# Performance work log

Hardware: AMD Instinct MI355X
Metric: run time of the kernel (lower is better)

## Reference

```python
import jax, jax.numpy as jnp
import numpy as np

SEQ, BATCH = 1024, 128
HIDDEN, EMBED, VOCAB = 2048, 512, 50257
EULER_STEP = 0.01
DIFFUSION = 0.001


def setup_inputs() -> dict:
    key = jax.random.key(0)
    ks = jax.random.split(key, 8)
    sqrt_k = 1.0 / np.sqrt(HIDDEN)
    inp = {
        "input_ids": jax.random.randint(ks[0], (SEQ, BATCH), 0, VOCAB),
        "h_init": jax.random.normal(ks[1], (BATCH, HIDDEN), dtype=jnp.float32),
        "embedding": jax.random.normal(ks[2], (VOCAB, EMBED), dtype=jnp.float32),
        "W_in": jax.random.uniform(ks[3], (HIDDEN, EMBED), jnp.float32, -sqrt_k, sqrt_k),
        "W_h": jax.random.uniform(ks[4], (HIDDEN, HIDDEN), jnp.float32, -sqrt_k, sqrt_k),
        "bias": jax.random.uniform(ks[5], (HIDDEN,), jnp.float32, -sqrt_k, sqrt_k),
        "fc_w": jax.random.uniform(ks[6], (VOCAB, HIDDEN), jnp.float32, -sqrt_k, sqrt_k),
        "fc_b": jax.random.uniform(ks[7], (VOCAB,), jnp.float32, -sqrt_k, sqrt_k),
        "temperature": 1,
    }
    return inp


def reference(input_ids, h_init, embedding, W_in, W_h, bias, fc_w, fc_b, temperature):
    # embed: [S, B, E]
    x = embedding[input_ids]
    # precompute input projection for all steps: [S, B, H]
    xin = jnp.einsum("sbe,he->sbh", x, W_in) + bias
    # effective antisymmetric transition matrix with diffusion
    W_eff = W_h - W_h.T - DIFFUSION * jnp.eye(HIDDEN, dtype=W_h.dtype)

    def step(h, u):
        # F.linear(h, W_eff) == h @ W_eff.T
        h = h + EULER_STEP * (h @ W_eff.T + u)
        return h, None

    h_final, _ = jax.lax.scan(step, h_init, xin)
    logits = (h_final @ fc_w.T + fc_b) / temperature
    return jax.nn.softmax(logits, axis=1)
```

## Files before the change

kernel.cpp:

```cpp
#include <hip/hip_runtime.h>
#include <hip/hip_bf16.h>


typedef _Float16 half8  __attribute__((ext_vector_type(8)));
typedef _Float16 half4h __attribute__((ext_vector_type(4)));
typedef float    f32x4  __attribute__((ext_vector_type(4)));
typedef unsigned int u32;

#define SEQ_    1024
#define BATCH_  128
#define HID_    2048
#define EMB_    512
#define VOC_    50257

__device__ __forceinline__ float decode_temp(const void* tp) {
  int bits = *(const int*)tp;
  float f = __int_as_float(bits);
  if (!(f > 1e-6f && f < 1e6f)) f = (float)bits;
  return f;
}

__device__ __forceinline__ void gl_lds16(const _Float16* g, _Float16* l) {
  __builtin_amdgcn_global_load_lds(
      (const __attribute__((address_space(1))) u32*)g,
      (__attribute__((address_space(3))) u32*)l, 16, 0, 0);
}

__global__ void gather_x_k(const int* __restrict__ ids, const float* __restrict__ embf,
                           _Float16* __restrict__ Xg) {
  const int sb = blockIdx.x * 4 + (threadIdx.x >> 6);
  const int lane = threadIdx.x & 63;
  const int s = sb >> 7, b = sb & 127;
  const int q = s >> 5, r = s & 31;
  const int id = ids[sb];
  const float* src = embf + (size_t)id * EMB_ + lane * 8;
  const f32x4 v0 = *(const f32x4*)src, v1 = *(const f32x4*)(src + 4);
  half8 h = { (_Float16)v0[0], (_Float16)v0[1], (_Float16)v0[2], (_Float16)v0[3],
              (_Float16)v1[0], (_Float16)v1[1], (_Float16)v1[2], (_Float16)v1[3] };
  const size_t drow = ((size_t)q * 128 + b) * 32 + r;
  *(half8*)(Xg + drow * EMB_ + lane * 8) = h;
}

__global__ void prep_R_k(const float* __restrict__ Wh, float* __restrict__ R32,
                         _Float16* __restrict__ R16, _Float16* __restrict__ RT0) {
  __shared__ float tA[64][65], tB[64][65];
  const int bi = blockIdx.y * 64, bj = blockIdx.x * 64;
  const int tx = threadIdx.x & 63, ty = threadIdx.x >> 6;
#pragma unroll
  for (int p = 0; p < 16; ++p) {
    int r = ty + p * 4;
    tA[r][tx] = Wh[(size_t)(bi + r) * HID_ + bj + tx];
    tB[r][tx] = Wh[(size_t)(bj + r) * HID_ + bi + tx];
  }
  __syncthreads();
#pragma unroll
  for (int p = 0; p < 16; ++p) {
    int r = ty + p * 4;
    int i = bi + r, j = bj + tx;
    float v = 0.64f * (tB[tx][r] - tA[r][tx]);
    if (i == j) v = -6.4e-4f;
    size_t idx = (size_t)i * HID_ + j;
    R32[idx] = v;
    R16[idx] = (_Float16)v;
    RT0[idx] = (_Float16)((i == j) ? v : -v);
  }
}

__global__ void copy_win_qt_k(const float* __restrict__ Win, _Float16* __restrict__ QT) {
  int t = blockIdx.x * 256 + threadIdx.x;
  int n = t / (EMB_ / 4), c4 = (t % (EMB_ / 4)) * 4;
  const f32x4 v = *(const f32x4*)(Win + (size_t)n * EMB_ + c4);
  half4h h = { (_Float16)v[0], (_Float16)v[1], (_Float16)v[2], (_Float16)v[3] };
  *(half4h*)(QT + (size_t)n * 16384 + 31 * EMB_ + c4) = h;
}

__global__ void transpose_f2h_k(const float* __restrict__ src, int ldsrc,
                                _Float16* __restrict__ dst, int lddst) {
  __shared__ float t[64][68];
  const int x0 = blockIdx.x * 64, y0 = blockIdx.y * 64;
  const int tid = threadIdx.x;
  const int xc = (tid & 15) * 4, ry = tid >> 4;
#pragma unroll
  for (int p = 0; p < 4; ++p) {
    int row = ry + p * 16;
    const f32x4 v = *(const f32x4*)(src + (size_t)(y0 + row) * ldsrc + x0 + xc);
    *(f32x4*)&t[row][xc] = v;
  }
  __syncthreads();
#pragma unroll
  for (int p = 0; p < 4; ++p) {
    int r2 = ry + p * 16;
    half4h h = { (_Float16)t[xc][r2], (_Float16)t[xc + 1][r2],
                 (_Float16)t[xc + 2][r2], (_Float16)t[xc + 3][r2] };
    *(half4h*)(dst + (size_t)(x0 + r2) * lddst + y0 + xc) = h;
  }
}

__global__ void transpose_q_k(const _Float16* __restrict__ Qst, int firstslot,
                              _Float16* __restrict__ QT) {
  __shared__ _Float16 t[64][72];
  const int slot = firstslot + blockIdx.z;
  const _Float16* src = Qst + (size_t)slot * (EMB_ * HID_);
  const int dc0 = (31 - slot) * EMB_;
  const int x0 = blockIdx.x * 64, y0 = blockIdx.y * 64;
  const int tid = threadIdx.x;
  const int xc = (tid & 7) * 8, ry = tid >> 3;
#pragma unroll
  for (int p = 0; p < 2; ++p) {
    int row = ry + p * 32;
    *(half8*)&t[row][xc] = *(const half8*)(src + (size_t)(y0 + row) * HID_ + x0 + xc);
  }
  __syncthreads();
#pragma unroll
  for (int p = 0; p < 2; ++p) {
    int r2 = ry + p * 32;
    half8 h = { t[xc][r2],     t[xc + 1][r2], t[xc + 2][r2], t[xc + 3][r2],
                t[xc + 4][r2], t[xc + 5][r2], t[xc + 6][r2], t[xc + 7][r2] };
    *(half8*)(QT + (size_t)(x0 + r2) * 16384 + dc0 + y0 + xc) = h;
  }
}

__global__ void gvec_part_k(const float* __restrict__ g, const float* __restrict__ R32,
                            float* __restrict__ gp) {
  const int j = blockIdx.x * 256 + threadIdx.x;
  const int i0 = blockIdx.y * 64;
  float s = 0.f;
#pragma unroll 4
  for (int i = 0; i < 64; ++i) s += g[i0 + i] * R32[(size_t)(i0 + i) * HID_ + j];
  gp[(size_t)blockIdx.y * HID_ + j] = s;
}
__global__ void gvec_red_k(const float* __restrict__ g, const float* __restrict__ gp,
                           float* __restrict__ gout) {
  const int j = blockIdx.x * 256 + threadIdx.x;
  float s = 0.f;
#pragma unroll
  for (int ib = 0; ib < 32; ++ib) s += gp[(size_t)ib * HID_ + j];
  gout[j] = 2.f * g[j] + s * (1.0f / 64.0f);
}

template<int BM, int BN, int BK, int WM, int WN, int ASRC, int BSRC, int EPI, int PAIR>
__global__ __launch_bounds__(256) void gemm_k(
    const void* __restrict__ Ap, int lda,
    const void* __restrict__ Bp, int ldb,
    int K, int Ntot, int ldc,
    float* __restrict__ o32, _Float16* __restrict__ o16,
    const float* __restrict__ auxA, const float* __restrict__ auxB,
    const _Float16* __restrict__ aux16,
    const float* __restrict__ vecf, const void* __restrict__ tptr) {
  __shared__ alignas(16) _Float16 At[BM][BK];
  __shared__ alignas(16) _Float16 Bts[BN][BK];
  constexpr int MF = WM / 16, NF = WN / 16, WNB = BN / WN;
  const int tid = threadIdx.x, lane = tid & 63, w = tid >> 6;
  const int wm0 = (w / WNB) * WM, wn0 = (w % WNB) * WN;
  const int bn0 = blockIdx.x * BN;
  const int bm0 = blockIdx.y * BM;
  const int pair = bm0 >> 7;
  const int rloc = bm0 & 127;

  size_t Aoff = 0;
  if constexpr (EPI == 2) Aoff = (size_t)blockIdx.z * 128 * 16384;

  f32x4 acc[MF][NF];
#pragma unroll
  for (int mf = 0; mf < MF; ++mf)
#pragma unroll
    for (int nf = 0; nf < NF; ++nf) acc[mf][nf] = (f32x4){0.f, 0.f, 0.f, 0.f};

  for (int k0 = 0; k0 < K; k0 += BK) {
    if constexpr (ASRC == 0) {
      const _Float16* Ag = (const _Float16*)Ap + Aoff + (size_t)k0;
      const int abase = PAIR ? (pair * 256 + rloc) : bm0;
#pragma unroll
      for (int i = 0; i < BM / 32; ++i) {
        const int rowb = (i * 4 + w) * 8;
        const int row = rowb + (lane >> 3);
        const int cf = (lane & 7) ^ (row & 7);
        gl_lds16(Ag + (size_t)(abase + row) * lda + cf * 8, &At[rowb][0]);
      }
    } else {
      const float* Ag = (const float*)Ap;
      constexpr int CH = BK / 4;
#pragma unroll
      for (int c = 0; c < (BM * CH) / 256; ++c) {
        int t = tid + c * 256;
        int row = t / CH, kc = t % CH;
        int arow = PAIR ? (pair * 256 + rloc + row) : (bm0 + row);
        f32x4 v = *(const f32x4*)(Ag + (size_t)arow * lda + k0 + kc * 4);
        int col = (((kc >> 1) ^ (row & 7)) << 3) + ((kc & 1) << 2);
        *(half4h*)&At[row][col] =
            (half4h){ (_Float16)v[0], (_Float16)v[1], (_Float16)v[2], (_Float16)v[3] };
      }
    }
    if constexpr (BSRC == 0) {
      const _Float16* Bg = (const _Float16*)Bp + (size_t)k0;
#pragma unroll
      for (int i = 0; i < BN / 32; ++i) {
        const int rowb = (i * 4 + w) * 8;
        const int row = rowb + (lane >> 3);
        const int cf = (lane & 7) ^ (row & 7);
        gl_lds16(Bg + (size_t)(bn0 + row) * ldb + cf * 8, &Bts[rowb][0]);
      }
    } else {
      const float* Bg = (const float*)Bp;
      constexpr int CH = BK / 4;
#pragma unroll
      for (int c = 0; c < (BN * CH) / 256; ++c) {
        int t = tid + c * 256;
        int row = t / CH, kc = t % CH;
        int gr = bn0 + row;
        half4h h = { (_Float16)0.f, (_Float16)0.f, (_Float16)0.f, (_Float16)0.f };
        if (gr < Ntot) {
          f32x4 v = *(const f32x4*)(Bg + (size_t)gr * ldb + k0 + kc * 4);
          h = (half4h){ (_Float16)v[0], (_Float16)v[1], (_Float16)v[2], (_Float16)v[3] };
        }
        int col = (((kc >> 1) ^ (row & 7)) << 3) + ((kc & 1) << 2);
        *(half4h*)&Bts[row][col] = h;
      }
    }
    __syncthreads();
#pragma unroll
    for (int kk = 0; kk < BK; kk += 32) {
      const int kb = kk + ((lane >> 4) << 3);
      half8 a[MF], b[NF];
#pragma unroll
      for (int mf = 0; mf < MF; ++mf) {
        const int row = wm0 + mf * 16 + (lane & 15);
        a[mf] = *(const half8*)&At[row][((kb >> 3) ^ (row & 7)) << 3];
      }
#pragma unroll
      for (int nf = 0; nf < NF; ++nf) {
        const int row = wn0 + nf * 16 + (lane & 15);
        b[nf] = *(const half8*)&Bts[row][((kb >> 3) ^ (row & 7)) << 3];
      }
#pragma unroll
      for (int mf = 0; mf < MF; ++mf)
#pragma unroll
        for (int nf = 0; nf < NF; ++nf)
          acc[mf][nf] = __builtin_amdgcn_mfma_f32_16x16x32_f16(a[mf], b[nf], acc[mf][nf], 0, 0, 0);
    }
    __syncthreads();
  }

  float invT = 1.0f;
  if constexpr (EPI == 4) invT = 1.0f / decode_temp(tptr);
  constexpr size_t BS = (size_t)BATCH_ * HID_;
#pragma unroll
  for (int mf = 0; mf < MF; ++mf)
#pragma unroll
    for (int nf = 0; nf < NF; ++nf) {
      const int col = bn0 + wn0 + nf * 16 + (lane & 15);
      const int r0 = wm0 + mf * 16 + ((lane >> 4) << 2);
#pragma unroll
      for (int r = 0; r < 4; ++r) {
        const int row = r0 + r;
        const float x = acc[mf][nf][r];
        if constexpr (EPI == 0) {
          size_t idx = (size_t)(bm0 + row) * ldc + col;
          float val = x * (1.0f / 64.0f) + 2.0f * auxA[idx];
          o32[idx] = val;
          o16[idx] = (_Float16)val;
        } else if constexpr (EPI == 1) {
          size_t idx = (size_t)(bm0 + row) * ldc + col;
          o16[idx] = (_Float16)(x * (1.0f / 64.0f) + (float)aux16[idx]);
        } else if constexpr (EPI == 2) {
          size_t idx = (size_t)row * ldc + col;
          o32[(size_t)blockIdx.z * BS + idx] = 0.01f * (x + vecf[col]);
        } else if constexpr (EPI == 3) {
          if constexpr (PAIR) {
            size_t off = (size_t)(rloc + row) * ldc + col;
            o32[(size_t)pair * BS + off] =
                x * (1.0f / 64.0f) + auxA[(size_t)pair * 2 * BS + off]
                                   + auxA[((size_t)pair * 2 + 1) * BS + off];
          } else {
            size_t idx = (size_t)(bm0 + row) * ldc + col;
            o32[idx] = x * (1.0f / 64.0f) + auxA[idx] + auxB[idx];
          }
        } else {
          if (col < Ntot)
            o32[(size_t)(bm0 + row) * ldc + col] = (x + vecf[col]) * invT;
        }
      }
    }
}

__global__ void softmax_k(const float* __restrict__ lg, float* __restrict__ out) {
  const int row = blockIdx.x;
  const float* lr = lg + (size_t)row * VOC_;
  float* orow = out + (size_t)row * VOC_;
  __shared__ float red[8];
  const int tid = threadIdx.x, lane = tid & 63, wid = tid >> 6;
  float m = -1e30f;
  for (int i = tid; i < VOC_; i += 256) m = fmaxf(m, lr[i]);
  for (int off = 32; off > 0; off >>= 1) m = fmaxf(m, __shfl_down(m, off, 64));
  if (lane == 0) red[wid] = m;
  __syncthreads();
  if (tid == 0) {
    float mm = red[0];
    for (int i = 1; i < 4; ++i) mm = fmaxf(mm, red[i]);
    red[4] = mm;
  }
  __syncthreads();
  const float bmax = red[4];
  float s = 0.f;
  for (int i = tid; i < VOC_; i += 256) s += __expf(lr[i] - bmax);
  for (int off = 32; off > 0; off >>= 1) s += __shfl_down(s, off, 64);
  if (lane == 0) red[wid] = s;
  __syncthreads();
  if (tid == 0) red[5] = red[0] + red[1] + red[2] + red[3];
  __syncthreads();
  const float inv = 1.0f / red[5];
  for (int i = tid; i < VOC_; i += 256) orow[i] = __expf(lr[i] - bmax) * inv;
}

extern "C" void kernel_launch(void* const* d_in, const int* in_sizes, int n_in,
                              void* d_out, int out_size, void* d_ws, size_t ws_size,
                              hipStream_t stream) {
  const int*   ids  = (const int*)d_in[0];
  const float* h0   = (const float*)d_in[1];
  const float* embf = (const float*)d_in[2];
  const float* Win  = (const float*)d_in[3];
  const float* Wh   = (const float*)d_in[4];
  const float* bias = (const float*)d_in[5];
  const float* fcw  = (const float*)d_in[6];
  const float* fcb  = (const float*)d_in[7];
  const void*  temp = d_in[8];
  float* out = (float*)d_out;

  char* w = (char*)d_ws;
  size_t o = 0;
  auto alloc = [&](size_t bytes) { char* p = w + o; o += (bytes + 255) & ~(size_t)255; return p; };

  _Float16* Xg   = (_Float16*)alloc((size_t)SEQ_ * BATCH_ * EMB_ * 2);
  float*    logits = (float*)Xg;
  float*    S    = (float*)alloc((size_t)32 * BATCH_ * HID_ * 4);
  float*    R32  = (float*)alloc((size_t)HID_ * HID_ * 4);
  _Float16* R16[2];
  R16[0] = (_Float16*)alloc((size_t)HID_ * HID_ * 2);
  R16[1] = (_Float16*)alloc((size_t)HID_ * HID_ * 2);
  _Float16* RTp[10];
  for (int i = 0; i < 10; ++i) RTp[i] = (_Float16*)alloc((size_t)HID_ * HID_ * 2);
  _Float16* Qst = (_Float16*)alloc((size_t)32 * EMB_ * HID_ * 2);
  _Float16* QT  = (_Float16*)alloc((size_t)HID_ * 16384 * 2);
  float* TA = (float*)alloc((size_t)16 * BATCH_ * HID_ * 4);
  float* TB = (float*)alloc((size_t)8 * BATCH_ * HID_ * 4);
  float* gp = (float*)alloc((size_t)32 * HID_ * 4);
  float* g[2];
  g[0] = (float*)alloc(HID_ * 4);
  g[1] = (float*)alloc(HID_ * 4);
  if (ws_size < o) return;

  const size_t QSLOT = (size_t)EMB_ * HID_;

  gather_x_k<<<SEQ_ * BATCH_ / 4, 256, 0, stream>>>(ids, embf, Xg);
  prep_R_k<<<dim3(32, 32), 256, 0, stream>>>(Wh, R32, R16[0], RTp[0]);
  transpose_f2h_k<<<dim3(EMB_ / 64, HID_ / 64), 256, 0, stream>>>(Win, EMB_, Qst, HID_);
  copy_win_qt_k<<<(HID_ * EMB_ / 4) / 256, 256, 0, stream>>>(Win, QT);

  for (int j = 0; j < 5; ++j) {
    const int nb = 1 << j;
    if (j < 3)
      gemm_k<64, 64, 64, 32, 32, 0, 0, 1, 0>
          <<<dim3(32, nb * 8), 256, 0, stream>>>(
          Qst, HID_, RTp[j], HID_, HID_, HID_, HID_,
          nullptr, Qst + (size_t)nb * QSLOT, nullptr, nullptr, Qst, nullptr, nullptr);
    else
      gemm_k<128, 128, 64, 64, 64, 0, 0, 1, 0>
          <<<dim3(16, nb * 4), 256, 0, stream>>>(
          Qst, HID_, RTp[j], HID_, HID_, HID_, HID_,
          nullptr, Qst + (size_t)nb * QSLOT, nullptr, nullptr, Qst, nullptr, nullptr);
    transpose_q_k<<<dim3(32, 8, nb), 256, 0, stream>>>(Qst, nb, QT);
    const float* gin = (j == 0) ? bias : g[(j + 1) & 1];
    gvec_part_k<<<dim3(8, 32), 256, 0, stream>>>(gin, R32, gp);
    gvec_red_k<<<8, 256, 0, stream>>>(gin, gp, g[j & 1]);
    gemm_k<64, 64, 64, 32, 32, 0, 0, 0, 0>
        <<<dim3(32, 32), 256, 0, stream>>>(
        R16[j & 1], HID_, RTp[j], HID_, HID_, HID_, HID_,
        R32, R16[(j & 1) ^ 1], R32, nullptr, nullptr, nullptr, nullptr);
    transpose_f2h_k<<<dim3(32, 32), 256, 0, stream>>>(R32, HID_, RTp[j + 1], HID_);
  }
  for (int j = 5; j < 9; ++j) {
    gemm_k<64, 64, 64, 32, 32, 0, 0, 0, 0>
        <<<dim3(32, 32), 256, 0, stream>>>(
        R16[j & 1], HID_, RTp[j], HID_, HID_, HID_, HID_,
        R32, R16[(j & 1) ^ 1], R32, nullptr, nullptr, nullptr, nullptr);
    transpose_f2h_k<<<dim3(32, 32), 256, 0, stream>>>(R32, HID_, RTp[j + 1], HID_);
  }

  gemm_k<128, 128, 64, 64, 64, 0, 0, 2, 0>
      <<<dim3(16, 1, 32), 256, 0, stream>>>(
      Xg, 16384, QT, 16384, 16384, HID_, HID_,
      S, nullptr, nullptr, nullptr, nullptr, g[0], nullptr);

  gemm_k<64, 64, 64, 32, 32, 1, 0, 3, 0>
      <<<dim3(32, 2), 256, 0, stream>>>(
      h0, HID_, RTp[5], HID_, HID_, HID_, HID_,
      S, nullptr, h0, S, nullptr, nullptr, nullptr);

  const float* tin = S;
  float* tout = TA;
  int pairs = 16;
  for (int l = 1; l <= 5; ++l) {
    gemm_k<64, 64, 64, 32, 32, 1, 0, 3, 1>
        <<<dim3(32, pairs * 2), 256, 0, stream>>>(
        tin, HID_, RTp[4 + l], HID_, HID_, HID_, HID_,
        tout, nullptr, tin, nullptr, nullptr, nullptr, nullptr);
    tin = tout;
    tout = (tout == TA) ? TB : TA;
    pairs >>= 1;
  }
  const float* H = tin;

  gemm_k<128, 128, 64, 64, 64, 1, 1, 4, 0>
      <<<dim3((VOC_ + 127) / 128, 1), 256, 0, stream>>>(
      H, HID_, fcw, HID_, HID_, VOC_, VOC_,
      logits, nullptr, nullptr, nullptr, nullptr, fcb, temp);

  softmax_k<<<BATCH_, 256, 0, stream>>>(logits, out);
}
```

Before: 2.081 ms.

## Fuse Q-propagation and R-squaring GEMMs with in-epilogue transposed stores

Q-slot propagation and the R matrix squaring are merged into one GEMM launch per doubling step. Its epilogue writes the transposed fp16 outputs (QT and the next RT) through shared memory, which removes the separate transpose_q_k and transpose_f2h_k kernels and their extra global round trips. R squaring now uses 128x128 tiles instead of 64x64. The big 16384-K S GEMM is split along K into two halves with a separate reduce kernel to add parallelism. The costs are an extra partial-sum buffer, extra reduce traffic, and a serialized four-pass shared-memory epilogue.

New measurement: 2.283 ms. +9.7%, slower.

```diff
diff --git a/kernel.cpp b/kernel.cpp
--- a/kernel.cpp
+++ b/kernel.cpp
@@ -12,6 +12,7 @@
 #define HID_    2048
 #define EMB_    512
 #define VOC_    50257
+#define QSLOT_  ((size_t)EMB_ * HID_)
 
 __device__ __forceinline__ float decode_temp(const void* tp) {
   int bits = *(const int*)tp;
@@ -96,30 +97,6 @@
   }
 }
 
-__global__ void transpose_q_k(const _Float16* __restrict__ Qst, int firstslot,
-                              _Float16* __restrict__ QT) {
-  __shared__ _Float16 t[64][72];
-  const int slot = firstslot + blockIdx.z;
-  const _Float16* src = Qst + (size_t)slot * (EMB_ * HID_);
-  const int dc0 = (31 - slot) * EMB_;
-  const int x0 = blockIdx.x * 64, y0 = blockIdx.y * 64;
-  const int tid = threadIdx.x;
-  const int xc = (tid & 7) * 8, ry = tid >> 3;
-#pragma unroll
-  for (int p = 0; p < 2; ++p) {
-    int row = ry + p * 32;
-    *(half8*)&t[row][xc] = *(const half8*)(src + (size_t)(y0 + row) * HID_ + x0 + xc);
-  }
-  __syncthreads();
-#pragma unroll
-  for (int p = 0; p < 2; ++p) {
-    int r2 = ry + p * 32;
-    half8 h = { t[xc][r2],     t[xc + 1][r2], t[xc + 2][r2], t[xc + 3][r2],
-                t[xc + 4][r2], t[xc + 5][r2], t[xc + 6][r2], t[xc + 7][r2] };
-    *(half8*)(QT + (size_t)(x0 + r2) * 16384 + dc0 + y0 + xc) = h;
-  }
-}
-
 __global__ void gvec_part_k(const float* __restrict__ g, const float* __restrict__ R32,
                             float* __restrict__ gp) {
   const int j = blockIdx.x * 256 + threadIdx.x;
@@ -138,17 +115,31 @@
   gout[j] = 2.f * g[j] + s * (1.0f / 64.0f);
 }
 
+__global__ void reduce_s_k(const float* __restrict__ P0, const float* __restrict__ P1,
+                           const float* __restrict__ g, float* __restrict__ S) {
+  const size_t t = (size_t)blockIdx.x * 256 + threadIdx.x;
+  const size_t i = t * 4;
+  const int col = (int)(i & 2047);
+  f32x4 a = *(const f32x4*)(P0 + i), b = *(const f32x4*)(P1 + i);
+  f32x4 r;
+#pragma unroll
+  for (int k = 0; k < 4; ++k) r[k] = 0.01f * (a[k] + b[k] + g[col + k]);
+  *(f32x4*)(S + i) = r;
+}
+
 template<int BM, int BN, int BK, int WM, int WN, int ASRC, int BSRC, int EPI, int PAIR>
 __global__ __launch_bounds__(256) void gemm_k(
     const void* __restrict__ Ap, int lda,
     const void* __restrict__ Bp, int ldb,
-    int K, int Ntot, int ldc,
-    float* __restrict__ o32, _Float16* __restrict__ o16,
+    int K, int Ntot, int ldc, int Mq, int nb,
+    float* __restrict__ o32, _Float16* __restrict__ o16b, _Float16* __restrict__ o16c,
+    _Float16* __restrict__ QTp,
     const float* __restrict__ auxA, const float* __restrict__ auxB,
     const _Float16* __restrict__ aux16,
     const float* __restrict__ vecf, const void* __restrict__ tptr) {
   __shared__ alignas(16) _Float16 At[BM][BK];
   __shared__ alignas(16) _Float16 Bts[BN][BK];
+  __shared__ float tpad[(EPI == 6) ? 64 * 65 : 1];
   constexpr int MF = WM / 16, NF = WN / 16, WNB = BN / WN;
   const int tid = threadIdx.x, lane = tid & 63, w = tid >> 6;
   const int wm0 = (w / WNB) * WM, wn0 = (w % WNB) * WN;
@@ -156,9 +147,7 @@
   const int bm0 = blockIdx.y * BM;
   const int pair = bm0 >> 7;
   const int rloc = bm0 & 127;
-
-  size_t Aoff = 0;
-  if constexpr (EPI == 2) Aoff = (size_t)blockIdx.z * 128 * 16384;
+  const int kz = (EPI == 5) ? blockIdx.z * 8192 : 0;
 
   f32x4 acc[MF][NF];
 #pragma unroll
@@ -168,14 +157,19 @@
 
   for (int k0 = 0; k0 < K; k0 += BK) {
     if constexpr (ASRC == 0) {
-      const _Float16* Ag = (const _Float16*)Ap + Aoff + (size_t)k0;
-      const int abase = PAIR ? (pair * 256 + rloc) : bm0;
+      const _Float16* Ag;
+      if constexpr (EPI == 6)
+        Ag = (bm0 < Mq) ? (aux16 + (size_t)bm0 * lda)
+                        : ((const _Float16*)Ap + (size_t)(bm0 - Mq) * lda);
+      else
+        Ag = (const _Float16*)Ap + (size_t)(PAIR ? pair * 256 + rloc : bm0) * lda;
+      Ag += (size_t)(k0 + kz);
 #pragma unroll
       for (int i = 0; i < BM / 32; ++i) {
         const int rowb = (i * 4 + w) * 8;
         const int row = rowb + (lane >> 3);
         const int cf = (lane & 7) ^ (row & 7);
-        gl_lds16(Ag + (size_t)(abase + row) * lda + cf * 8, &At[rowb][0]);
+        gl_lds16(Ag + (size_t)row * lda + cf * 8, &At[rowb][0]);
       }
     } else {
       const float* Ag = (const float*)Ap;
@@ -192,7 +186,7 @@
       }
     }
     if constexpr (BSRC == 0) {
-      const _Float16* Bg = (const _Float16*)Bp + (size_t)k0;
+      const _Float16* Bg = (const _Float16*)Bp + (size_t)(k0 + kz);
 #pragma unroll
       for (int i = 0; i < BN / 32; ++i) {
         const int rowb = (i * 4 + w) * 8;
@@ -244,43 +238,102 @@
   float invT = 1.0f;
   if constexpr (EPI == 4) invT = 1.0f / decode_temp(tptr);
   constexpr size_t BS = (size_t)BATCH_ * HID_;
-#pragma unroll
-  for (int mf = 0; mf < MF; ++mf)
-#pragma unroll
-    for (int nf = 0; nf < NF; ++nf) {
-      const int col = bn0 + wn0 + nf * 16 + (lane & 15);
-      const int r0 = wm0 + mf * 16 + ((lane >> 4) << 2);
-#pragma unroll
-      for (int r = 0; r < 4; ++r) {
-        const int row = r0 + r;
-        const float x = acc[mf][nf][r];
-        if constexpr (EPI == 0) {
-          size_t idx = (size_t)(bm0 + row) * ldc + col;
-          float val = x * (1.0f / 64.0f) + 2.0f * auxA[idx];
-          o32[idx] = val;
-          o16[idx] = (_Float16)val;
-        } else if constexpr (EPI == 1) {
-          size_t idx = (size_t)(bm0 + row) * ldc + col;
-          o16[idx] = (_Float16)(x * (1.0f / 64.0f) + (float)aux16[idx]);
-        } else if constexpr (EPI == 2) {
-          size_t idx = (size_t)row * ldc + col;
-          o32[(size_t)blockIdx.z * BS + idx] = 0.01f * (x + vecf[col]);
-        } else if constexpr (EPI == 3) {
-          if constexpr (PAIR) {
-            size_t off = (size_t)(rloc + row) * ldc + col;
-            o32[(size_t)pair * BS + off] =
-                x * (1.0f / 64.0f) + auxA[(size_t)pair * 2 * BS + off]
-                                   + auxA[((size_t)pair * 2 + 1) * BS + off];
+  const int quad4 = (lane >> 4) << 2;
+
+  if constexpr (EPI == 6) {
+    const bool isQ = (bm0 < Mq);
+    _Float16* oq = (_Float16*)aux16 + (size_t)nb * QSLOT_;
+#pragma unroll
+    for (int mf = 0; mf < MF; ++mf)
+#pragma unroll
+      for (int nf = 0; nf < NF; ++nf) {
+        const int col = bn0 + wn0 + nf * 16 + (lane & 15);
+        const int r0 = wm0 + mf * 16 + quad4;
+#pragma unroll
+        for (int r = 0; r < 4; ++r) {
+          const int rowloc = r0 + r;
+          float val;
+          if (isQ) {
+            size_t idx = (size_t)(bm0 + rowloc) * ldc + col;
+            val = acc[mf][nf][r] * (1.0f / 64.0f) + (float)aux16[idx];
+            oq[idx] = (_Float16)val;
           } else {
-            size_t idx = (size_t)(bm0 + row) * ldc + col;
-            o32[idx] = x * (1.0f / 64.0f) + auxA[idx] + auxB[idx];
+            size_t idx = (size_t)(bm0 - Mq + rowloc) * ldc + col;
+            val = acc[mf][nf][r] * (1.0f / 64.0f) + 2.0f * auxA[idx];
+            o32[idx] = val;
+            o16b[idx] = (_Float16)val;
           }
+          acc[mf][nf][r] = val;
+        }
+      }
+#pragma unroll 1
+    for (int qq = 0; qq < 4; ++qq) {
+      if (w == qq) {
+#pragma unroll
+        for (int mf = 0; mf < MF; ++mf)
+#pragma unroll
+          for (int nf = 0; nf < NF; ++nf)
+#pragma unroll
+            for (int r = 0; r < 4; ++r)
+              tpad[(mf * 16 + quad4 + r) * 65 + nf * 16 + (lane & 15)] = acc[mf][nf][r];
+      }
+      __syncthreads();
+      {
+        const int qm = (qq >> 1) * 64, qn = (qq & 1) * 64;
+        _Float16* dst;
+        int ldd;
+        size_t dbase;
+        if (isQ) {
+          const int arow = bm0 + qm;
+          const int slot_out = nb + (arow >> 9);
+          dbase = (size_t)(31 - slot_out) * 512 + (arow & 511);
+          dst = QTp; ldd = 16384;
         } else {
-          if (col < Ntot)
-            o32[(size_t)(bm0 + row) * ldc + col] = (x + vecf[col]) * invT;
+          dbase = (size_t)(bm0 - Mq) + qm;
+          dst = o16c; ldd = HID_;
         }
-      }
+#pragma unroll
+        for (int pass = 0; pass < 2; ++pass) {
+          const int jj = (tid >> 3) + pass * 32;
+          const int iic = (tid & 7) * 8;
+          half8 hv;
+#pragma unroll
+          for (int t = 0; t < 8; ++t) hv[t] = (_Float16)tpad[(iic + t) * 65 + jj];
+          *(half8*)(dst + (size_t)(bn0 + qn + jj) * ldd + dbase + iic) = hv;
+        }
+      }
+      __syncthreads();
     }
+  } else {
+#pragma unroll
+    for (int mf = 0; mf < MF; ++mf)
+#pragma unroll
+      for (int nf = 0; nf < NF; ++nf) {
+        const int col = bn0 + wn0 + nf * 16 + (lane & 15);
+        const int r0 = wm0 + mf * 16 + quad4;
+#pragma unroll
+        for (int r = 0; r < 4; ++r) {
+          const int row = r0 + r;
+          const float x = acc[mf][nf][r];
+          if constexpr (EPI == 3) {
+            if constexpr (PAIR) {
+              size_t off = (size_t)(rloc + row) * ldc + col;
+              o32[(size_t)pair * BS + off] =
+                  x * (1.0f / 64.0f) + auxA[(size_t)pair * 2 * BS + off]
+                                     + auxA[((size_t)pair * 2 + 1) * BS + off];
+            } else {
+              size_t idx = (size_t)(bm0 + row) * ldc + col;
+              o32[idx] = x * (1.0f / 64.0f) + auxA[idx] + auxB[idx];
+            }
+          } else if constexpr (EPI == 5) {
+            o32[(size_t)blockIdx.z * 8388608 + (size_t)(bm0 + row) * ldc + col] = x;
+          } else {
+            if (col < Ntot)
+              o32[(size_t)(bm0 + row) * ldc + col] = (x + vecf[col]) * invT;
+          }
+        }
+      }
+  }
 }
 
 __global__ void softmax_k(const float* __restrict__ lg, float* __restrict__ out) {
@@ -330,17 +383,19 @@
   size_t o = 0;
   auto alloc = [&](size_t bytes) { char* p = w + o; o += (bytes + 255) & ~(size_t)255; return p; };
 
-  _Float16* Xg   = (_Float16*)alloc((size_t)SEQ_ * BATCH_ * EMB_ * 2);
+  _Float16* Xg = (_Float16*)alloc((size_t)SEQ_ * BATCH_ * EMB_ * 2);
   float*    logits = (float*)Xg;
-  float*    S    = (float*)alloc((size_t)32 * BATCH_ * HID_ * 4);
-  float*    R32  = (float*)alloc((size_t)HID_ * HID_ * 4);
+  float*    S   = (float*)alloc((size_t)32 * BATCH_ * HID_ * 4);
+  float*    R32 = (float*)alloc((size_t)HID_ * HID_ * 4);
   _Float16* R16[2];
   R16[0] = (_Float16*)alloc((size_t)HID_ * HID_ * 2);
   R16[1] = (_Float16*)alloc((size_t)HID_ * HID_ * 2);
   _Float16* RTp[10];
   for (int i = 0; i < 10; ++i) RTp[i] = (_Float16*)alloc((size_t)HID_ * HID_ * 2);
-  _Float16* Qst = (_Float16*)alloc((size_t)32 * EMB_ * HID_ * 2);
-  _Float16* QT  = (_Float16*)alloc((size_t)HID_ * 16384 * 2);
+  _Float16* Qst = (_Float16*)alloc((size_t)32 * QSLOT_ * 2);
+  float* P0 = (float*)Qst;
+  float* P1 = P0 + (size_t)4096 * 2048;
+  _Float16* QT = (_Float16*)alloc((size_t)HID_ * 16384 * 2);
   float* TA = (float*)alloc((size_t)16 * BATCH_ * HID_ * 4);
   float* TB = (float*)alloc((size_t)8 * BATCH_ * HID_ * 4);
   float* gp = (float*)alloc((size_t)32 * HID_ * 4);
@@ -349,8 +404,6 @@
   g[1] = (float*)alloc(HID_ * 4);
   if (ws_size < o) return;
 
-  const size_t QSLOT = (size_t)EMB_ * HID_;
-
   gather_x_k<<<SEQ_ * BATCH_ / 4, 256, 0, stream>>>(ids, embf, Xg);
   prep_R_k<<<dim3(32, 32), 256, 0, stream>>>(Wh, R32, R16[0], RTp[0]);
   transpose_f2h_k<<<dim3(EMB_ / 64, HID_ / 64), 256, 0, stream>>>(Win, EMB_, Qst, HID_);
@@ -358,43 +411,33 @@
 
   for (int j = 0; j < 5; ++j) {
     const int nb = 1 << j;
-    if (j < 3)
-      gemm_k<64, 64, 64, 32, 32, 0, 0, 1, 0>
-          <<<dim3(32, nb * 8), 256, 0, stream>>>(
-          Qst, HID_, RTp[j], HID_, HID_, HID_, HID_,
-          nullptr, Qst + (size_t)nb * QSLOT, nullptr, nullptr, Qst, nullptr, nullptr);
-    else
-      gemm_k<128, 128, 64, 64, 64, 0, 0, 1, 0>
-          <<<dim3(16, nb * 4), 256, 0, stream>>>(
-          Qst, HID_, RTp[j], HID_, HID_, HID_, HID_,
-          nullptr, Qst + (size_t)nb * QSLOT, nullptr, nullptr, Qst, nullptr, nullptr);
-    transpose_q_k<<<dim3(32, 8, nb), 256, 0, stream>>>(Qst, nb, QT);
     const float* gin = (j == 0) ? bias : g[(j + 1) & 1];
     gvec_part_k<<<dim3(8, 32), 256, 0, stream>>>(gin, R32, gp);
     gvec_red_k<<<8, 256, 0, stream>>>(gin, gp, g[j & 1]);
-    gemm_k<64, 64, 64, 32, 32, 0, 0, 0, 0>
-        <<<dim3(32, 32), 256, 0, stream>>>(
-        R16[j & 1], HID_, RTp[j], HID_, HID_, HID_, HID_,
-        R32, R16[(j & 1) ^ 1], R32, nullptr, nullptr, nullptr, nullptr);
-    transpose_f2h_k<<<dim3(32, 32), 256, 0, stream>>>(R32, HID_, RTp[j + 1], HID_);
+    gemm_k<128, 128, 64, 64, 64, 0, 0, 6, 0>
+        <<<dim3(16, nb * 4 + 16), 256, 0, stream>>>(
+        R16[j & 1], HID_, RTp[j], HID_, HID_, HID_, HID_, nb * 512, nb,
+        R32, R16[(j & 1) ^ 1], RTp[j + 1], QT,
+        R32, nullptr, Qst, nullptr, nullptr);
   }
   for (int j = 5; j < 9; ++j) {
-    gemm_k<64, 64, 64, 32, 32, 0, 0, 0, 0>
-        <<<dim3(32, 32), 256, 0, stream>>>(
-        R16[j & 1], HID_, RTp[j], HID_, HID_, HID_, HID_,
-        R32, R16[(j & 1) ^ 1], R32, nullptr, nullptr, nullptr, nullptr);
-    transpose_f2h_k<<<dim3(32, 32), 256, 0, stream>>>(R32, HID_, RTp[j + 1], HID_);
-  }
-
-  gemm_k<128, 128, 64, 64, 64, 0, 0, 2, 0>
-      <<<dim3(16, 1, 32), 256, 0, stream>>>(
-      Xg, 16384, QT, 16384, 16384, HID_, HID_,
-      S, nullptr, nullptr, nullptr, nullptr, g[0], nullptr);
+    gemm_k<128, 128, 64, 64, 64, 0, 0, 6, 0>
+        <<<dim3(16, 16), 256, 0, stream>>>(
+        R16[j & 1], HID_, RTp[j], HID_, HID_, HID_, HID_, 0, 0,
+        R32, R16[(j & 1) ^ 1], RTp[j + 1], nullptr,
+        R32, nullptr, nullptr, nullptr, nullptr);
+  }
+
+  gemm_k<128, 128, 64, 64, 64, 0, 0, 5, 0>
+      <<<dim3(16, 32, 2), 256, 0, stream>>>(
+      Xg, 16384, QT, 16384, 8192, HID_, HID_, 0, 0,
+      P0, nullptr, nullptr, nullptr, nullptr, nullptr, nullptr, nullptr, nullptr);
+  reduce_s_k<<<8192, 256, 0, stream>>>(P0, P1, g[0], S);
 
   gemm_k<64, 64, 64, 32, 32, 1, 0, 3, 0>
       <<<dim3(32, 2), 256, 0, stream>>>(
-      h0, HID_, RTp[5], HID_, HID_, HID_, HID_,
-      S, nullptr, h0, S, nullptr, nullptr, nullptr);
+      h0, HID_, RTp[5], HID_, HID_, HID_, HID_, 0, 0,
+      S, nullptr, nullptr, nullptr, h0, S, nullptr, nullptr, nullptr);
 
   const float* tin = S;
   float* tout = TA;
@@ -402,8 +445,8 @@
   for (int l = 1; l <= 5; ++l) {
     gemm_k<64, 64, 64, 32, 32, 1, 0, 3, 1>
         <<<dim3(32, pairs * 2), 256, 0, stream>>>(
-        tin, HID_, RTp[4 + l], HID_, HID_, HID_, HID_,
-        tout, nullptr, tin, nullptr, nullptr, nullptr, nullptr);
+        tin, HID_, RTp[4 + l], HID_, HID_, HID_, HID_, 0, 0,
+        tout, nullptr, nullptr, nullptr, tin, nullptr, nullptr, nullptr, nullptr);
     tin = tout;
     tout = (tout == TA) ? TB : TA;
     pairs >>= 1;
@@ -412,8 +455,8 @@
 
   gemm_k<128, 128, 64, 64, 64, 1, 1, 4, 0>
       <<<dim3((VOC_ + 127) / 128, 1), 256, 0, stream>>>(
-      H, HID_, fcw, HID_, HID_, VOC_, VOC_,
-      logits, nullptr, nullptr, nullptr, nullptr, fcb, temp);
+      H, HID_, fcw, HID_, HID_, VOC_, VOC_, 0, 0,
+      logits, nullptr, nullptr, nullptr, nullptr, nullptr, nullptr, fcb, temp);
 
   softmax_k<<<BATCH_, 256, 0, stream>>>(logits, out);
 }
```
